# Kernel optimization log

Hardware: AMD Instinct MI355X
Metric: run time of the kernel (lower is better)

## Reference

```python
import math
import jax, jax.numpy as jnp
import numpy as np

N_HEAD = 12
LN_EPS = 1e-5

def _gelu(x):
    # NewGELU: tanh approximation
    c = math.sqrt(2.0 / math.pi)
    return 0.5 * x * (1.0 + jnp.tanh(c * (x + 0.044715 * x ** 3)))

def _ln(x, w, b):
    m = x.mean(-1, keepdims=True)
    v = x.var(-1, keepdims=True)
    return (x - m) / jnp.sqrt(v + LN_EPS) * w + b

def setup_inputs() -> dict:
    key = jax.random.key(0)
    ks = jax.random.split(key, 8)
    L, C, V, BS = 12, 768, 30522, 1024
    B, T = 4, 1024
    std = 0.02
    inp = {
        'idx': jax.random.randint(ks[0], (B, T), 0, V),
        'wte': jax.random.normal(ks[1], (V, C), jnp.float32) * std,
        'wpe': jax.random.normal(ks[2], (BS, C), jnp.float32) * std,
        'ln1_w': jnp.ones((L, C), jnp.float32),
        'ln1_b': jnp.zeros((L, C), jnp.float32),
        'attn_w': jax.random.normal(ks[3], (L, 3 * C, C), jnp.float32) * std,
        'attn_b': jnp.zeros((L, 3 * C), jnp.float32),
        'proj_w': jax.random.normal(ks[4], (L, C, C), jnp.float32) * (std / math.sqrt(2 * L)),
        'proj_b': jnp.zeros((L, C), jnp.float32),
        'ln2_w': jnp.ones((L, C), jnp.float32),
        'ln2_b': jnp.zeros((L, C), jnp.float32),
        'fc_w': jax.random.normal(ks[5], (L, 4 * C, C), jnp.float32) * std,
        'fc_b': jnp.zeros((L, 4 * C), jnp.float32),
        'mproj_w': jax.random.normal(ks[6], (L, C, 4 * C), jnp.float32) * (std / math.sqrt(2 * L)),
        'mproj_b': jnp.zeros((L, C), jnp.float32),
        'lnf_w': jnp.ones((C,), jnp.float32),
        'lnf_b': jnp.zeros((C,), jnp.float32),
        'lm_head_w': jax.random.normal(ks[7], (V, C), jnp.float32) * std,
    }
    return inp

def reference(idx, wte, wpe, ln1_w, ln1_b, attn_w, attn_b, proj_w, proj_b,
              ln2_w, ln2_b, fc_w, fc_b, mproj_w, mproj_b, lnf_w, lnf_b, lm_head_w):
    B, T = idx.shape
    C = wte.shape[1]
    H = N_HEAD
    D = C // H
    scale = 1.0 / math.sqrt(D)
    x = wte[idx] + wpe[:T][None]  # [B,T,C], drop is identity (p=0)

    def block(x, p):
        l1w, l1b, aw, ab, pw, pb, l2w, l2b, fw, fb, mw, mb = p
        h = _ln(x, l1w, l1b)
        qkv = jnp.einsum('btc,ec->bte', h, aw) + ab  # [B,T,3C]
        q, k, v = jnp.split(qkv, 3, axis=-1)
        q = q.reshape(B, T, H, D)
        k = k.reshape(B, T, H, D)
        v = v.reshape(B, T, H, D)
        att = jnp.einsum('bthd,bshd->bhts', q, k) * scale  # [B,H,T,T]
        att = jax.nn.softmax(att, axis=-1)  # mask=None: full attention
        y = jnp.einsum('bhts,bshd->bthd', att, v).reshape(B, T, C)
        x = x + jnp.einsum('btc,oc->bto', y, pw) + pb
        h = _gelu(jnp.einsum('btc,fc->btf', _ln(x, l2w, l2b), fw) + fb)
        x = x + jnp.einsum('btf,cf->btc', h, mw) + mb
        return x, None

    x, _ = jax.lax.scan(block, x, (ln1_w, ln1_b, attn_w, attn_b, proj_w, proj_b,
                                   ln2_w, ln2_b, fc_w, fc_b, mproj_w, mproj_b))
    x = _ln(x, lnf_w, lnf_b)
    logits = jnp.einsum('btc,vc->btv', x, lm_head_w)  # [B,T,V]
    return logits
```

## Files before the change

### kernel.cpp

```cpp
#include <hip/hip_runtime.h>
#include <hip/hip_bf16.h>
#include <math.h>

typedef __attribute__((ext_vector_type(8))) short short8;
typedef __attribute__((ext_vector_type(4))) float f32x4;

typedef unsigned short u16;

__device__ __forceinline__ u16 f2bf(float f) {
    union { float f; unsigned int u; } v; v.f = f;
    unsigned int u = v.u;
    unsigned int r = (u + 0x7fffu + ((u >> 16) & 1u)) >> 16;
    return (u16)r;
}
__device__ __forceinline__ float bf2f(u16 u) {
    union { unsigned int u; float f; } v; v.u = ((unsigned int)u) << 16;
    return v.f;
}

__device__ __forceinline__ void gload16(const void* g, void* l) {
    __builtin_amdgcn_global_load_lds(
        (const __attribute__((address_space(1))) void*)g,
        (__attribute__((address_space(3))) void*)l, 16, 0, 0);
}

__global__ __launch_bounds__(256) void castw_kernel(const float* __restrict__ src,
                                                    u16* __restrict__ dst,
                                                    long n, long npad) {
    long i = ((long)blockIdx.x * 256 + threadIdx.x) * 4;
    const long stride = (long)gridDim.x * 1024;
    for (; i < npad; i += stride) {
        ushort4 o;
        if (i < n) {
            float4 v = *reinterpret_cast<const float4*>(src + i);
            o.x = f2bf(v.x); o.y = f2bf(v.y); o.z = f2bf(v.z); o.w = f2bf(v.w);
        } else {
            o = make_ushort4(0, 0, 0, 0);
        }
        *reinterpret_cast<ushort4*>(dst + i) = o;
    }
}

__global__ __launch_bounds__(256) void embed_kernel(const int* __restrict__ idx,
                                                    const float* __restrict__ wte,
                                                    const float* __restrict__ wpe,
                                                    float* __restrict__ x) {
    const int row = blockIdx.x;
    const int tid = threadIdx.x;
    const int t = row & 1023;
    const int tok = idx[row];
    const float* we = wte + (size_t)tok * 768;
    const float* pe = wpe + (size_t)t * 768;
    float* xr = x + (size_t)row * 768;
    xr[tid]       = we[tid]       + pe[tid];
    xr[tid + 256] = we[tid + 256] + pe[tid + 256];
    xr[tid + 512] = we[tid + 512] + pe[tid + 512];
}

__global__ __launch_bounds__(256) void ln_kernel(const float* __restrict__ x,
                                                 const float* __restrict__ w,
                                                 const float* __restrict__ b,
                                                 u16* __restrict__ out) {
    const int wid = threadIdx.x >> 6, lane = threadIdx.x & 63;
    const int row = blockIdx.x * 4 + wid;
    const float* xr = x + (size_t)row * 768;
    const float4 v0 = *reinterpret_cast<const float4*>(xr + lane * 4);
    const float4 v1 = *reinterpret_cast<const float4*>(xr + 256 + lane * 4);
    const float4 v2 = *reinterpret_cast<const float4*>(xr + 512 + lane * 4);
    float s = v0.x + v0.y + v0.z + v0.w + v1.x + v1.y + v1.z + v1.w
            + v2.x + v2.y + v2.z + v2.w;
    float q = v0.x * v0.x + v0.y * v0.y + v0.z * v0.z + v0.w * v0.w
            + v1.x * v1.x + v1.y * v1.y + v1.z * v1.z + v1.w * v1.w
            + v2.x * v2.x + v2.y * v2.y + v2.z * v2.z + v2.w * v2.w;
    #pragma unroll
    for (int off = 32; off >= 1; off >>= 1) {
        s += __shfl_xor(s, off);
        q += __shfl_xor(q, off);
    }
    const float mean = s * (1.f / 768.f);
    const float var = q * (1.f / 768.f) - mean * mean;
    const float rstd = rsqrtf(var + 1e-5f);
    u16* orow = out + (size_t)row * 768;
    #pragma unroll
    for (int seg = 0; seg < 3; seg++) {
        const float4 v = seg == 0 ? v0 : (seg == 1 ? v1 : v2);
        const float4 wv = *reinterpret_cast<const float4*>(w + seg * 256 + lane * 4);
        const float4 bv = *reinterpret_cast<const float4*>(b + seg * 256 + lane * 4);
        ushort4 ov;
        ov.x = f2bf((v.x - mean) * rstd * wv.x + bv.x);
        ov.y = f2bf((v.y - mean) * rstd * wv.y + bv.y);
        ov.z = f2bf((v.z - mean) * rstd * wv.z + bv.z);
        ov.w = f2bf((v.w - mean) * rstd * wv.w + bv.w);
        *reinterpret_cast<ushort4*>(orow + seg * 256 + lane * 4) = ov;
    }
}

template<int EPI, int ORDER>
__global__ __launch_bounds__(512) void gemm_big(
        const u16* __restrict__ A, int lda,
        const u16* __restrict__ B, int ldb,
        const float* __restrict__ bias,
        void* __restrict__ Cout, int ldc,
        int N, int K, int nmt) {
    __shared__ __align__(16) u16 lds[2][384 * 32];
    const int tid = threadIdx.x;
    const int lane = tid & 63, wid = tid >> 6;
    const int nwg = gridDim.x;
    const int o = blockIdx.x;
    const int wg = (o & 7) * (nwg >> 3) + (o >> 3);
    int m0, n0;
    if (ORDER == 0) { m0 = (wg % nmt) * 256; n0 = (wg / nmt) * 128; }
    else            { n0 = (wg % nmt) * 128; m0 = (wg / nmt) * 256; }

    const int wm = (wid >> 1) * 64, wn = (wid & 1) * 64;
    const int l16 = lane & 15;
    const int qid = lane >> 4;
    const int xq8 = ((qid ^ (l16 & 3)) * 8);

    const int ar = tid >> 2, aq = (tid & 3) ^ (ar & 3);
    const size_t a_src0 = (size_t)(m0 + ar) * lda + aq * 8;
    const size_t a_src1 = (size_t)(m0 + ar + 128) * lda + aq * 8;
    const size_t b_src = (size_t)(n0 + ar) * ldb + aq * 8;

    f32x4 acc[4][4];
    #pragma unroll
    for (int i = 0; i < 4; i++)
        #pragma unroll
        for (int j = 0; j < 4; j++)
            acc[i][j] = (f32x4){0.f, 0.f, 0.f, 0.f};

    const int nk = K >> 5;
    gload16(A + a_src0, lds[0] + tid * 8);
    gload16(A + a_src1, lds[0] + tid * 8 + 4096);
    gload16(B + b_src,  lds[0] + tid * 8 + 8192);

    for (int t = 0; t < nk; ++t) {
        if (t + 1 < nk) {
            u16* buf = lds[(t + 1) & 1];
            const int k0 = (t + 1) << 5;
            gload16(A + a_src0 + k0, buf + tid * 8);
            gload16(A + a_src1 + k0, buf + tid * 8 + 4096);
            gload16(B + b_src + k0,  buf + tid * 8 + 8192);
            asm volatile("s_waitcnt vmcnt(3)" ::: "memory");
        } else {
            asm volatile("s_waitcnt vmcnt(0)" ::: "memory");
        }
        __builtin_amdgcn_s_barrier();
        asm volatile("" ::: "memory");
        const u16* As = lds[t & 1];
        const u16* Bs = lds[t & 1] + 8192;
        short8 af[4], bf[4];
        #pragma unroll
        for (int i = 0; i < 4; i++) {
            af[i] = *reinterpret_cast<const short8*>(&As[(wm + i * 16 + l16) * 32 + xq8]);
            bf[i] = *reinterpret_cast<const short8*>(&Bs[(wn + i * 16 + l16) * 32 + xq8]);
        }
        #pragma unroll
        for (int mi = 0; mi < 4; mi++)
            #pragma unroll
            for (int ni = 0; ni < 4; ni++)
                acc[mi][ni] = __builtin_amdgcn_mfma_f32_16x16x32_bf16(af[mi], bf[ni], acc[mi][ni], 0, 0, 0);
        asm volatile("" ::: "memory");
        __builtin_amdgcn_s_barrier();
    }

    if (EPI == 3) {
        float* ct = reinterpret_cast<float*>(&lds[0][0]) + wid * 1088;
        const int rw = (lane >> 4) * 4;
        const int rr = lane >> 2;
        const int rc = (lane & 3) * 16;
        #pragma unroll
        for (int mi = 0; mi < 4; mi++) {
            asm volatile("" ::: "memory");
            #pragma unroll
            for (int ni = 0; ni < 4; ni++)
                #pragma unroll
                for (int j = 0; j < 4; j++)
                    ct[(rw + j) * 68 + ni * 16 + l16] = acc[mi][ni][j];
            asm volatile("" ::: "memory");
            const int m = m0 + wm + mi * 16 + rr;
            const int nb = n0 + wn + rc;
            float* crow = (float*)Cout + (size_t)m * ldc + nb;
            #pragma unroll
            for (int q = 0; q < 4; q++) {
                const f32x4 v = *reinterpret_cast<const f32x4*>(&ct[rr * 68 + rc + q * 4]);
                if (nb + q * 4 + 3 < N) {
                    *reinterpret_cast<f32x4*>(crow + q * 4) = v;
                } else {
                    #pragma unroll
                    for (int e = 0; e < 4; e++)
                        if (nb + q * 4 + e < N) crow[q * 4 + e] = v[e];
                }
            }
            asm volatile("" ::: "memory");
            __builtin_amdgcn_s_barrier();
        }
    } else {
        const int cb = n0 + wn + l16;
        const int rb = m0 + wm + (lane >> 4) * 4;
        #pragma unroll
        for (int ni = 0; ni < 4; ni++) {
            const int n = cb + ni * 16;
            const float bv = bias[n];
            #pragma unroll
            for (int mi = 0; mi < 4; mi++) {
                #pragma unroll
                for (int j = 0; j < 4; j++) {
                    const int m = rb + mi * 16 + j;
                    float v = acc[mi][ni][j] + bv;
                    if (EPI == 0) {
                        ((u16*)Cout)[(size_t)m * ldc + n] = f2bf(v);
                    } else {
                        const float t = tanhf(0.7978845608028654f * (v + 0.044715f * v * v * v));
                        ((u16*)Cout)[(size_t)m * ldc + n] = f2bf(0.5f * v * (1.f + t));
                    }
                }
            }
        }
    }
}

__global__ __launch_bounds__(256) void gemm_splitk(
        const u16* __restrict__ A, int lda,
        const u16* __restrict__ B, int ldb,
        const float* __restrict__ bias,
        int ldc, int Kp, int nmt, int ntiles,
        float* __restrict__ resid) {
    __shared__ __align__(16) u16 lds[2][2][128 * 32];
    const int tid = threadIdx.x;
    const int lane = tid & 63, wid = tid >> 6;
    const int nwg = gridDim.x;
    const int o = blockIdx.x;
    const int wg = (o & 7) * (nwg >> 3) + (o >> 3);
    const int tile = wg % ntiles;
    const int ks = wg / ntiles;
    const int m0 = (tile % nmt) * 128, n0 = (tile / nmt) * 128;
    const int koff = ks * Kp;

    const int wm = (wid >> 1) * 64, wn = (wid & 1) * 64;
    const int l16 = lane & 15;
    const int qid = lane >> 4;
    const int xq8 = ((qid ^ (l16 & 3)) * 8);

    const int r0 = tid >> 2, q0 = (tid & 3) ^ (r0 & 3);
    const size_t a_src0 = (size_t)(m0 + r0) * lda + koff + q0 * 8;
    const size_t a_src1 = (size_t)(m0 + r0 + 64) * lda + koff + q0 * 8;
    const size_t b_src0 = (size_t)(n0 + r0) * ldb + koff + q0 * 8;
    const size_t b_src1 = (size_t)(n0 + r0 + 64) * ldb + koff + q0 * 8;

    f32x4 acc[4][4];
    #pragma unroll
    for (int i = 0; i < 4; i++)
        #pragma unroll
        for (int j = 0; j < 4; j++)
            acc[i][j] = (f32x4){0.f, 0.f, 0.f, 0.f};

    const int nk = Kp >> 5;
    gload16(A + a_src0, lds[0][0] + tid * 8);
    gload16(A + a_src1, lds[0][0] + tid * 8 + 2048);
    gload16(B + b_src0, lds[0][1] + tid * 8);
    gload16(B + b_src1, lds[0][1] + tid * 8 + 2048);

    for (int t = 0; t < nk; ++t) {
        if (t + 1 < nk) {
            u16* Ap = lds[(t + 1) & 1][0];
            u16* Bp = lds[(t + 1) & 1][1];
            const int k0 = (t + 1) << 5;
            gload16(A + a_src0 + k0, Ap + tid * 8);
            gload16(A + a_src1 + k0, Ap + tid * 8 + 2048);
            gload16(B + b_src0 + k0, Bp + tid * 8);
            gload16(B + b_src1 + k0, Bp + tid * 8 + 2048);
            asm volatile("s_waitcnt vmcnt(4)" ::: "memory");
        } else {
            asm volatile("s_waitcnt vmcnt(0)" ::: "memory");
        }
        __builtin_amdgcn_s_barrier();
        asm volatile("" ::: "memory");
        const u16* As = lds[t & 1][0];
        const u16* Bs = lds[t & 1][1];
        short8 af[4], bf[4];
        #pragma unroll
        for (int i = 0; i < 4; i++) {
            af[i] = *reinterpret_cast<const short8*>(&As[(wm + i * 16 + l16) * 32 + xq8]);
            bf[i] = *reinterpret_cast<const short8*>(&Bs[(wn + i * 16 + l16) * 32 + xq8]);
        }
        #pragma unroll
        for (int mi = 0; mi < 4; mi++)
            #pragma unroll
            for (int ni = 0; ni < 4; ni++)
                acc[mi][ni] = __builtin_amdgcn_mfma_f32_16x16x32_bf16(af[mi], bf[ni], acc[mi][ni], 0, 0, 0);
        asm volatile("" ::: "memory");
        __builtin_amdgcn_s_barrier();
    }

    const int cb = n0 + wn + l16;
    const int rb = m0 + wm + (lane >> 4) * 4;
    #pragma unroll
    for (int ni = 0; ni < 4; ni++) {
        const int n = cb + ni * 16;
        const float bv = (ks == 0) ? bias[n] : 0.f;
        #pragma unroll
        for (int mi = 0; mi < 4; mi++) {
            #pragma unroll
            for (int j = 0; j < 4; j++) {
                const int m = rb + mi * 16 + j;
                atomicAdd(&resid[(size_t)m * ldc + n], acc[mi][ni][j] + bv);
            }
        }
    }
}

template<int EPI>
__global__ __launch_bounds__(256, 2) void gemm_bt(
        const u16* __restrict__ A, int lda,
        const float* __restrict__ B, int ldb,
        const float* __restrict__ bias,
        void* __restrict__ Cout, int ldc,
        int M, int N, int K,
        float* __restrict__ resid) {
    __shared__ __align__(16) u16 As[128][40];
    __shared__ __align__(16) u16 Bs[128][40];
    const int tid = threadIdx.x;
    const int lane = tid & 63, wid = tid >> 6;
    const int m0 = blockIdx.y * 128, n0 = blockIdx.x * 128;
    const int wm = (wid >> 1) * 64, wn = (wid & 1) * 64;
    const int l16 = lane & 15, lk = (lane >> 4) * 8;

    f32x4 acc[4][4];
    #pragma unroll
    for (int i = 0; i < 4; i++)
        #pragma unroll
        for (int j = 0; j < 4; j++)
            acc[i][j] = (f32x4){0.f, 0.f, 0.f, 0.f};

    for (int k0 = 0; k0 < K; k0 += 32) {
        #pragma unroll
        for (int p = 0; p < 2; p++) {
            const int e = p * 256 + tid;
            const int r = e >> 2, c = e & 3;
            uint4 v = *reinterpret_cast<const uint4*>(A + (size_t)(m0 + r) * lda + k0 + c * 8);
            *reinterpret_cast<uint4*>(&As[r][c * 8]) = v;
        }
        #pragma unroll
        for (int p = 0; p < 4; p++) {
            const int e = p * 256 + tid;
            const int r = e >> 3, c = e & 7;
            float4 v = make_float4(0.f, 0.f, 0.f, 0.f);
            if (n0 + r < N)
                v = *reinterpret_cast<const float4*>(B + (size_t)(n0 + r) * ldb + k0 + c * 4);
            ushort4 hv;
            hv.x = f2bf(v.x); hv.y = f2bf(v.y); hv.z = f2bf(v.z); hv.w = f2bf(v.w);
            *reinterpret_cast<ushort4*>(&Bs[r][c * 4]) = hv;
        }
        __syncthreads();
        short8 af[4], bfr[4];
        #pragma unroll
        for (int i = 0; i < 4; i++) {
            af[i]  = *reinterpret_cast<const short8*>(&As[wm + i * 16 + l16][lk]);
            bfr[i] = *reinterpret_cast<const short8*>(&Bs[wn + i * 16 + l16][lk]);
        }
        #pragma unroll
        for (int mi = 0; mi < 4; mi++)
            #pragma unroll
            for (int ni = 0; ni < 4; ni++)
                acc[mi][ni] = __builtin_amdgcn_mfma_f32_16x16x32_bf16(af[mi], bfr[ni], acc[mi][ni], 0, 0, 0);
        __syncthreads();
    }

    const int cb = n0 + wn + l16;
    const int rb = m0 + wm + (lane >> 4) * 4;
    #pragma unroll
    for (int ni = 0; ni < 4; ni++) {
        const int n = cb + ni * 16;
        if (n >= N) continue;
        float bv = 0.f;
        if (EPI != 3) bv = bias[n];
        #pragma unroll
        for (int mi = 0; mi < 4; mi++) {
            #pragma unroll
            for (int j = 0; j < 4; j++) {
                const int m = rb + mi * 16 + j;
                float v = acc[mi][ni][j] + bv;
                if (EPI == 0) {
                    ((u16*)Cout)[(size_t)m * ldc + n] = f2bf(v);
                } else if (EPI == 1) {
                    resid[(size_t)m * ldc + n] += v;
                } else if (EPI == 2) {
                    const float t = tanhf(0.7978845608028654f * (v + 0.044715f * v * v * v));
                    ((u16*)Cout)[(size_t)m * ldc + n] = f2bf(0.5f * v * (1.f + t));
                } else {
                    ((float*)Cout)[(size_t)m * ldc + n] = v;
                }
            }
        }
    }
}

__global__ __launch_bounds__(256, 2) void attn_mfma_kernel(const u16* __restrict__ qkv,
                                                           u16* __restrict__ y) {
    __shared__ __align__(16) u16 Qs[64][72];
    __shared__ __align__(16) u16 Ks[2][64][72];
    __shared__ __align__(16) u16 Vt[2][64][72];
    __shared__ __align__(16) u16 Ps[4][16][72];

    const int tid = threadIdx.x;
    const int lane = tid & 63, wid = tid >> 6;
    const int l16 = lane & 15, lk = (lane >> 4) * 8;
    const int qt = blockIdx.x, h = blockIdx.y, b = blockIdx.z;

    const size_t base = (size_t)b * 1024 * 2304;
    const u16* qp = qkv + base + (size_t)(qt * 64) * 2304 + h * 64;
    const u16* kp = qkv + base + 768  + h * 64;
    const u16* vp = qkv + base + 1536 + h * 64;

    const int krr0 = tid >> 3, kc8_0 = tid & 7;
    const int krr1 = (tid + 256) >> 3, kc8_1 = tid & 7;
    const int vs0 = (tid >> 4) * 2, vdq0 = tid & 15;
    const int vs1 = ((tid + 256) >> 4) * 2, vdq1 = tid & 15;

    #pragma unroll
    for (int p = 0; p < 2; p++) {
        const int e = p * 256 + tid;
        const int rr = e >> 3, c8 = e & 7;
        *reinterpret_cast<uint4*>(&Qs[rr][c8 * 8]) =
            *reinterpret_cast<const uint4*>(qp + (size_t)rr * 2304 + c8 * 8);
    }
    uint4 kreg0, kreg1; ushort4 vr0a, vr0b, vr1a, vr1b;
    kreg0 = *reinterpret_cast<const uint4*>(kp + (size_t)krr0 * 2304 + kc8_0 * 8);
    kreg1 = *reinterpret_cast<const uint4*>(kp + (size_t)krr1 * 2304 + kc8_1 * 8);
    vr0a = *reinterpret_cast<const ushort4*>(vp + (size_t)vs0 * 2304 + vdq0 * 4);
    vr0b = *reinterpret_cast<const ushort4*>(vp + (size_t)(vs0 + 1) * 2304 + vdq0 * 4);
    vr1a = *reinterpret_cast<const ushort4*>(vp + (size_t)vs1 * 2304 + vdq1 * 4);
    vr1b = *reinterpret_cast<const ushort4*>(vp + (size_t)(vs1 + 1) * 2304 + vdq1 * 4);
    __syncthreads();

    short8 qf[2];
    #pragma unroll
    for (int kk = 0; kk < 2; kk++)
        qf[kk] = *reinterpret_cast<const short8*>(&Qs[wid * 16 + l16][kk * 32 + lk]);

    *reinterpret_cast<uint4*>(&Ks[0][krr0][kc8_0 * 8]) = kreg0;
    *reinterpret_cast<uint4*>(&Ks[0][krr1][kc8_1 * 8]) = kreg1;
    *reinterpret_cast<ushort2*>(&Vt[0][vdq0 * 4 + 0][vs0]) = make_ushort2(vr0a.x, vr0b.x);
    *reinterpret_cast<ushort2*>(&Vt[0][vdq0 * 4 + 1][vs0]) = make_ushort2(vr0a.y, vr0b.y);
    *reinterpret_cast<ushort2*>(&Vt[0][vdq0 * 4 + 2][vs0]) = make_ushort2(vr0a.z, vr0b.z);
    *reinterpret_cast<ushort2*>(&Vt[0][vdq0 * 4 + 3][vs0]) = make_ushort2(vr0a.w, vr0b.w);
    *reinterpret_cast<ushort2*>(&Vt[0][vdq1 * 4 + 0][vs1]) = make_ushort2(vr1a.x, vr1b.x);
    *reinterpret_cast<ushort2*>(&Vt[0][vdq1 * 4 + 1][vs1]) = make_ushort2(vr1a.y, vr1b.y);
    *reinterpret_cast<ushort2*>(&Vt[0][vdq1 * 4 + 2][vs1]) = make_ushort2(vr1a.z, vr1b.z);
    *reinterpret_cast<ushort2*>(&Vt[0][vdq1 * 4 + 3][vs1]) = make_ushort2(vr1a.w, vr1b.w);
    __syncthreads();

    f32x4 o_acc[4];
    #pragma unroll
    for (int i = 0; i < 4; i++) o_acc[i] = (f32x4){0.f, 0.f, 0.f, 0.f};
    float l_part[4] = {0.f, 0.f, 0.f, 0.f};

    for (int t = 0; t < 16; ++t) {
        const int cur = t & 1, nxt = cur ^ 1;
        if (t + 1 < 16) {
            const int s0 = (t + 1) * 64;
            kreg0 = *reinterpret_cast<const uint4*>(kp + (size_t)(s0 + krr0) * 2304 + kc8_0 * 8);
            kreg1 = *reinterpret_cast<const uint4*>(kp + (size_t)(s0 + krr1) * 2304 + kc8_1 * 8);
            vr0a = *reinterpret_cast<const ushort4*>(vp + (size_t)(s0 + vs0) * 2304 + vdq0 * 4);
            vr0b = *reinterpret_cast<const ushort4*>(vp + (size_t)(s0 + vs0 + 1) * 2304 + vdq0 * 4);
            vr1a = *reinterpret_cast<const ushort4*>(vp + (size_t)(s0 + vs1) * 2304 + vdq1 * 4);
            vr1b = *reinterpret_cast<const ushort4*>(vp + (size_t)(s0 + vs1 + 1) * 2304 + vdq1 * 4);
        }

        f32x4 sa[4];
        #pragma unroll
        for (int i = 0; i < 4; i++) sa[i] = (f32x4){0.f, 0.f, 0.f, 0.f};
        #pragma unroll
        for (int nj = 0; nj < 4; nj++) {
            #pragma unroll
            for (int kk = 0; kk < 2; kk++) {
                short8 kf = *reinterpret_cast<const short8*>(&Ks[cur][nj * 16 + l16][kk * 32 + lk]);
                sa[nj] = __builtin_amdgcn_mfma_f32_16x16x32_bf16(qf[kk], kf, sa[nj], 0, 0, 0);
            }
        }
        #pragma unroll
        for (int nj = 0; nj < 4; nj++) {
            #pragma unroll
            for (int r = 0; r < 4; r++) {
                const float pv = __expf(sa[nj][r] * 0.125f);
                l_part[r] += pv;
                Ps[wid][(lane >> 4) * 4 + r][nj * 16 + l16] = f2bf(pv);
            }
        }
        short8 pa[2];
        #pragma unroll
        for (int kk = 0; kk < 2; kk++)
            pa[kk] = *reinterpret_cast<const short8*>(&Ps[wid][l16][kk * 32 + lk]);
        #pragma unroll
        for (int nd = 0; nd < 4; nd++) {
            #pragma unroll
            for (int kk = 0; kk < 2; kk++) {
                short8 vf = *reinterpret_cast<const short8*>(&Vt[cur][nd * 16 + l16][kk * 32 + lk]);
                o_acc[nd] = __builtin_amdgcn_mfma_f32_16x16x32_bf16(pa[kk], vf, o_acc[nd], 0, 0, 0);
            }
        }

        if (t + 1 < 16) {
            *reinterpret_cast<uint4*>(&Ks[nxt][krr0][kc8_0 * 8]) = kreg0;
            *reinterpret_cast<uint4*>(&Ks[nxt][krr1][kc8_1 * 8]) = kreg1;
            *reinterpret_cast<ushort2*>(&Vt[nxt][vdq0 * 4 + 0][vs0]) = make_ushort2(vr0a.x, vr0b.x);
            *reinterpret_cast<ushort2*>(&Vt[nxt][vdq0 * 4 + 1][vs0]) = make_ushort2(vr0a.y, vr0b.y);
            *reinterpret_cast<ushort2*>(&Vt[nxt][vdq0 * 4 + 2][vs0]) = make_ushort2(vr0a.z, vr0b.z);
            *reinterpret_cast<ushort2*>(&Vt[nxt][vdq0 * 4 + 3][vs0]) = make_ushort2(vr0a.w, vr0b.w);
            *reinterpret_cast<ushort2*>(&Vt[nxt][vdq1 * 4 + 0][vs1]) = make_ushort2(vr1a.x, vr1b.x);
            *reinterpret_cast<ushort2*>(&Vt[nxt][vdq1 * 4 + 1][vs1]) = make_ushort2(vr1a.y, vr1b.y);
            *reinterpret_cast<ushort2*>(&Vt[nxt][vdq1 * 4 + 2][vs1]) = make_ushort2(vr1a.z, vr1b.z);
            *reinterpret_cast<ushort2*>(&Vt[nxt][vdq1 * 4 + 3][vs1]) = make_ushort2(vr1a.w, vr1b.w);
        }
        __syncthreads();
    }

    float inv[4];
    #pragma unroll
    for (int r = 0; r < 4; r++) {
        float s = l_part[r];
        #pragma unroll
        for (int off = 8; off >= 1; off >>= 1) s += __shfl_xor(s, off);
        inv[r] = 1.f / s;
    }
    const int rowb = b * 1024 + qt * 64 + wid * 16 + (lane >> 4) * 4;
    #pragma unroll
    for (int nd = 0; nd < 4; nd++) {
        const int col = h * 64 + nd * 16 + l16;
        #pragma unroll
        for (int r = 0; r < 4; r++) {
            y[(size_t)(rowb + r) * 768 + col] = f2bf(o_acc[nd][r] * inv[r]);
        }
    }
}

extern "C" void kernel_launch(void* const* d_in, const int* in_sizes, int n_in,
                              void* d_out, int out_size, void* d_ws, size_t ws_size,
                              hipStream_t stream) {
    (void)in_sizes; (void)n_in; (void)out_size;
    const int*   idx    = (const int*)d_in[0];
    const float* wte    = (const float*)d_in[1];
    const float* wpe    = (const float*)d_in[2];
    const float* ln1w   = (const float*)d_in[3];
    const float* ln1b   = (const float*)d_in[4];
    const float* attnw  = (const float*)d_in[5];
    const float* attnb  = (const float*)d_in[6];
    const float* projw  = (const float*)d_in[7];
    const float* projb  = (const float*)d_in[8];
    const float* ln2w   = (const float*)d_in[9];
    const float* ln2b   = (const float*)d_in[10];
    const float* fcw    = (const float*)d_in[11];
    const float* fcb    = (const float*)d_in[12];
    const float* mprojw = (const float*)d_in[13];
    const float* mprojb = (const float*)d_in[14];
    const float* lnfw   = (const float*)d_in[15];
    const float* lnfb   = (const float*)d_in[16];
    const float* lmw    = (const float*)d_in[17];
    float* out = (float*)d_out;

    char* p = (char*)d_ws;
    size_t used = 0;
    auto take = [&](size_t bytes) { char* q = p + used; used += (bytes + 255) & ~(size_t)255; return q; };
    float* x      = (float*)take((size_t)4096 * 768 * 4);
    u16*   a_bf   = (u16*)take((size_t)4096 * 768 * 2);
    u16*   qkv_bf = (u16*)take((size_t)4096 * 2304 * 2);
    u16*   hid_bf = (u16*)take((size_t)4096 * 3072 * 2);
    u16*   w_lm   = (u16*)take((size_t)30592 * 768 * 2);
    const bool castLm = used <= ws_size;
    u16*   w_attn = (u16*)take((size_t)12 * 2304 * 768 * 2);
    u16*   w_proj = (u16*)take((size_t)12 * 768 * 768 * 2);
    u16*   w_fc   = (u16*)take((size_t)12 * 3072 * 768 * 2);
    u16*   w_mprj = (u16*)take((size_t)12 * 768 * 3072 * 2);
    const bool castAll = used <= ws_size;

    embed_kernel<<<4096, 256, 0, stream>>>(idx, wte, wpe, x);

    if (castLm)
        castw_kernel<<<2048, 256, 0, stream>>>(lmw, w_lm, (long)30522 * 768, (long)30592 * 768);
    if (castAll) {
        castw_kernel<<<2048, 256, 0, stream>>>(attnw,  w_attn, (long)12 * 2304 * 768, (long)12 * 2304 * 768);
        castw_kernel<<<2048, 256, 0, stream>>>(projw,  w_proj, (long)12 * 768 * 768,  (long)12 * 768 * 768);
        castw_kernel<<<2048, 256, 0, stream>>>(fcw,    w_fc,   (long)12 * 3072 * 768, (long)12 * 3072 * 768);
        castw_kernel<<<2048, 256, 0, stream>>>(mprojw, w_mprj, (long)12 * 768 * 3072, (long)12 * 768 * 3072);
    }

    for (int l = 0; l < 12; l++) {
        ln_kernel<<<1024, 256, 0, stream>>>(x, ln1w + l * 768, ln1b + l * 768, a_bf);
        if (castAll) {
            gemm_big<0, 0><<<16 * 18, 512, 0, stream>>>(
                a_bf, 768, w_attn + (size_t)l * 2304 * 768, 768, attnb + l * 2304,
                (void*)qkv_bf, 2304, 2304, 768, 16);
        } else {
            gemm_bt<0><<<dim3(18, 32), 256, 0, stream>>>(
                a_bf, 768, attnw + (size_t)l * 2304 * 768, 768, attnb + l * 2304,
                (void*)qkv_bf, 2304, 4096, 2304, 768, nullptr);
        }
        attn_mfma_kernel<<<dim3(16, 12, 4), 256, 0, stream>>>(qkv_bf, a_bf);
        if (castAll) {
            gemm_splitk<<<192 * 2, 256, 0, stream>>>(
                a_bf, 768, w_proj + (size_t)l * 768 * 768, 768, projb + l * 768,
                768, 384, 32, 192, x);
        } else {
            gemm_bt<1><<<dim3(6, 32), 256, 0, stream>>>(
                a_bf, 768, projw + (size_t)l * 768 * 768, 768, projb + l * 768,
                nullptr, 768, 4096, 768, 768, x);
        }
        ln_kernel<<<1024, 256, 0, stream>>>(x, ln2w + l * 768, ln2b + l * 768, a_bf);
        if (castAll) {
            gemm_big<2, 0><<<16 * 24, 512, 0, stream>>>(
                a_bf, 768, w_fc + (size_t)l * 3072 * 768, 768, fcb + l * 3072,
                (void*)hid_bf, 3072, 3072, 768, 16);
            gemm_splitk<<<192 * 4, 256, 0, stream>>>(
                hid_bf, 3072, w_mprj + (size_t)l * 768 * 3072, 3072, mprojb + l * 768,
                768, 768, 32, 192, x);
        } else {
            gemm_bt<2><<<dim3(24, 32), 256, 0, stream>>>(
                a_bf, 768, fcw + (size_t)l * 3072 * 768, 768, fcb + l * 3072,
                (void*)hid_bf, 3072, 4096, 3072, 768, nullptr);
            gemm_bt<1><<<dim3(6, 32), 256, 0, stream>>>(
                hid_bf, 3072, mprojw + (size_t)l * 768 * 3072, 3072, mprojb + l * 768,
                nullptr, 768, 4096, 768, 3072, x);
        }
    }

    ln_kernel<<<1024, 256, 0, stream>>>(x, lnfw, lnfb, a_bf);
    if (castLm) {
        gemm_big<3, 1><<<16 * 239, 512, 0, stream>>>(
            a_bf, 768, w_lm, 768, nullptr, (void*)out, 30522, 30522, 768, 239);
    } else {
        gemm_bt<3><<<dim3(239, 32), 256, 0, stream>>>(
            a_bf, 768, lmw, 768, nullptr, (void*)out, 30522, 4096, 30522, 768, nullptr);
    }
}
```

Before: 3.039 ms.

## Widen attention tiles to 128 queries, retune GEMM LDS swizzle and padding

The attention kernel now processes 128 query rows per workgroup with 8 waves (512 threads), so each K/V tile loaded into LDS is shared by twice as many queries and global K/V traffic is halved. The GEMM kernels change the LDS XOR swizzle to key on row pairs instead of single rows, aimed at fewer bank conflicts with the 16x16x32 MFMA fragment reads. The EPI==3 staging stride goes from 68 to 76 floats, also to reduce bank conflicts. In exchange the attention grid has half as many workgroups (384), and larger blocks with more LDS may lower occupancy.

New measurement: 2.996 ms. No clear change (-1.4%).

```diff
diff --git a/kernel.cpp b/kernel.cpp
--- a/kernel.cpp
+++ b/kernel.cpp
@@ -115,9 +115,9 @@
     const int wm = (wid >> 1) * 64, wn = (wid & 1) * 64;
     const int l16 = lane & 15;
     const int qid = lane >> 4;
-    const int xq8 = ((qid ^ (l16 & 3)) * 8);
-
-    const int ar = tid >> 2, aq = (tid & 3) ^ (ar & 3);
+    const int xq8 = ((qid ^ ((l16 >> 1) & 3)) * 8);
+
+    const int ar = tid >> 2, aq = (tid & 3) ^ ((ar >> 1) & 3);
     const size_t a_src0 = (size_t)(m0 + ar) * lda + aq * 8;
     const size_t a_src1 = (size_t)(m0 + ar + 128) * lda + aq * 8;
     const size_t b_src = (size_t)(n0 + ar) * ldb + aq * 8;
@@ -165,7 +165,7 @@
     }
 
     if (EPI == 3) {
-        float* ct = reinterpret_cast<float*>(&lds[0][0]) + wid * 1088;
+        float* ct = reinterpret_cast<float*>(&lds[0][0]) + wid * 1216;
         const int rw = (lane >> 4) * 4;
         const int rr = lane >> 2;
         const int rc = (lane & 3) * 16;
@@ -176,14 +176,14 @@
             for (int ni = 0; ni < 4; ni++)
                 #pragma unroll
                 for (int j = 0; j < 4; j++)
-                    ct[(rw + j) * 68 + ni * 16 + l16] = acc[mi][ni][j];
+                    ct[(rw + j) * 76 + ni * 16 + l16] = acc[mi][ni][j];
             asm volatile("" ::: "memory");
             const int m = m0 + wm + mi * 16 + rr;
             const int nb = n0 + wn + rc;
             float* crow = (float*)Cout + (size_t)m * ldc + nb;
             #pragma unroll
             for (int q = 0; q < 4; q++) {
-                const f32x4 v = *reinterpret_cast<const f32x4*>(&ct[rr * 68 + rc + q * 4]);
+                const f32x4 v = *reinterpret_cast<const f32x4*>(&ct[rr * 76 + rc + q * 4]);
                 if (nb + q * 4 + 3 < N) {
                     *reinterpret_cast<f32x4*>(crow + q * 4) = v;
                 } else {
@@ -240,9 +240,9 @@
     const int wm = (wid >> 1) * 64, wn = (wid & 1) * 64;
     const int l16 = lane & 15;
     const int qid = lane >> 4;
-    const int xq8 = ((qid ^ (l16 & 3)) * 8);
-
-    const int r0 = tid >> 2, q0 = (tid & 3) ^ (r0 & 3);
+    const int xq8 = ((qid ^ ((l16 >> 1) & 3)) * 8);
+
+    const int r0 = tid >> 2, q0 = (tid & 3) ^ ((r0 >> 1) & 3);
     const size_t a_src0 = (size_t)(m0 + r0) * lda + koff + q0 * 8;
     const size_t a_src1 = (size_t)(m0 + r0 + 64) * lda + koff + q0 * 8;
     const size_t b_src0 = (size_t)(n0 + r0) * ldb + koff + q0 * 8;
@@ -396,12 +396,12 @@
     }
 }
 
-__global__ __launch_bounds__(256, 2) void attn_mfma_kernel(const u16* __restrict__ qkv,
+__global__ __launch_bounds__(512, 2) void attn_mfma_kernel(const u16* __restrict__ qkv,
                                                            u16* __restrict__ y) {
-    __shared__ __align__(16) u16 Qs[64][72];
+    __shared__ __align__(16) u16 Qs[128][72];
     __shared__ __align__(16) u16 Ks[2][64][72];
     __shared__ __align__(16) u16 Vt[2][64][72];
-    __shared__ __align__(16) u16 Ps[4][16][72];
+    __shared__ __align__(16) u16 Ps[8][16][72];
 
     const int tid = threadIdx.x;
     const int lane = tid & 63, wid = tid >> 6;
@@ -409,29 +409,24 @@
     const int qt = blockIdx.x, h = blockIdx.y, b = blockIdx.z;
 
     const size_t base = (size_t)b * 1024 * 2304;
-    const u16* qp = qkv + base + (size_t)(qt * 64) * 2304 + h * 64;
+    const u16* qp = qkv + base + (size_t)(qt * 128) * 2304 + h * 64;
     const u16* kp = qkv + base + 768  + h * 64;
     const u16* vp = qkv + base + 1536 + h * 64;
 
-    const int krr0 = tid >> 3, kc8_0 = tid & 7;
-    const int krr1 = (tid + 256) >> 3, kc8_1 = tid & 7;
-    const int vs0 = (tid >> 4) * 2, vdq0 = tid & 15;
-    const int vs1 = ((tid + 256) >> 4) * 2, vdq1 = tid & 15;
+    const int krr = tid >> 3, kc8 = tid & 7;
+    const int vs = (tid >> 4) * 2, vdq = tid & 15;
 
     #pragma unroll
     for (int p = 0; p < 2; p++) {
-        const int e = p * 256 + tid;
+        const int e = p * 512 + tid;
         const int rr = e >> 3, c8 = e & 7;
         *reinterpret_cast<uint4*>(&Qs[rr][c8 * 8]) =
             *reinterpret_cast<const uint4*>(qp + (size_t)rr * 2304 + c8 * 8);
     }
-    uint4 kreg0, kreg1; ushort4 vr0a, vr0b, vr1a, vr1b;
-    kreg0 = *reinterpret_cast<const uint4*>(kp + (size_t)krr0 * 2304 + kc8_0 * 8);
-    kreg1 = *reinterpret_cast<const uint4*>(kp + (size_t)krr1 * 2304 + kc8_1 * 8);
-    vr0a = *reinterpret_cast<const ushort4*>(vp + (size_t)vs0 * 2304 + vdq0 * 4);
-    vr0b = *reinterpret_cast<const ushort4*>(vp + (size_t)(vs0 + 1) * 2304 + vdq0 * 4);
-    vr1a = *reinterpret_cast<const ushort4*>(vp + (size_t)vs1 * 2304 + vdq1 * 4);
-    vr1b = *reinterpret_cast<const ushort4*>(vp + (size_t)(vs1 + 1) * 2304 + vdq1 * 4);
+    uint4 kreg; ushort4 vra, vrb;
+    kreg = *reinterpret_cast<const uint4*>(kp + (size_t)krr * 2304 + kc8 * 8);
+    vra = *reinterpret_cast<const ushort4*>(vp + (size_t)vs * 2304 + vdq * 4);
+    vrb = *reinterpret_cast<const ushort4*>(vp + (size_t)(vs + 1) * 2304 + vdq * 4);
     __syncthreads();
 
     short8 qf[2];
@@ -439,16 +434,11 @@
     for (int kk = 0; kk < 2; kk++)
         qf[kk] = *reinterpret_cast<const short8*>(&Qs[wid * 16 + l16][kk * 32 + lk]);
 
-    *reinterpret_cast<uint4*>(&Ks[0][krr0][kc8_0 * 8]) = kreg0;
-    *reinterpret_cast<uint4*>(&Ks[0][krr1][kc8_1 * 8]) = kreg1;
-    *reinterpret_cast<ushort2*>(&Vt[0][vdq0 * 4 + 0][vs0]) = make_ushort2(vr0a.x, vr0b.x);
-    *reinterpret_cast<ushort2*>(&Vt[0][vdq0 * 4 + 1][vs0]) = make_ushort2(vr0a.y, vr0b.y);
-    *reinterpret_cast<ushort2*>(&Vt[0][vdq0 * 4 + 2][vs0]) = make_ushort2(vr0a.z, vr0b.z);
-    *reinterpret_cast<ushort2*>(&Vt[0][vdq0 * 4 + 3][vs0]) = make_ushort2(vr0a.w, vr0b.w);
-    *reinterpret_cast<ushort2*>(&Vt[0][vdq1 * 4 + 0][vs1]) = make_ushort2(vr1a.x, vr1b.x);
-    *reinterpret_cast<ushort2*>(&Vt[0][vdq1 * 4 + 1][vs1]) = make_ushort2(vr1a.y, vr1b.y);
-    *reinterpret_cast<ushort2*>(&Vt[0][vdq1 * 4 + 2][vs1]) = make_ushort2(vr1a.z, vr1b.z);
-    *reinterpret_cast<ushort2*>(&Vt[0][vdq1 * 4 + 3][vs1]) = make_ushort2(vr1a.w, vr1b.w);
+    *reinterpret_cast<uint4*>(&Ks[0][krr][kc8 * 8]) = kreg;
+    *reinterpret_cast<ushort2*>(&Vt[0][vdq * 4 + 0][vs]) = make_ushort2(vra.x, vrb.x);
+    *reinterpret_cast<ushort2*>(&Vt[0][vdq * 4 + 1][vs]) = make_ushort2(vra.y, vrb.y);
+    *reinterpret_cast<ushort2*>(&Vt[0][vdq * 4 + 2][vs]) = make_ushort2(vra.z, vrb.z);
+    *reinterpret_cast<ushort2*>(&Vt[0][vdq * 4 + 3][vs]) = make_ushort2(vra.w, vrb.w);
     __syncthreads();
 
     f32x4 o_acc[4];
@@ -460,12 +450,9 @@
         const int cur = t & 1, nxt = cur ^ 1;
         if (t + 1 < 16) {
             const int s0 = (t + 1) * 64;
-            kreg0 = *reinterpret_cast<const uint4*>(kp + (size_t)(s0 + krr0) * 2304 + kc8_0 * 8);
-            kreg1 = *reinterpret_cast<const uint4*>(kp + (size_t)(s0 + krr1) * 2304 + kc8_1 * 8);
-            vr0a = *reinterpret_cast<const ushort4*>(vp + (size_t)(s0 + vs0) * 2304 + vdq0 * 4);
-            vr0b = *reinterpret_cast<const ushort4*>(vp + (size_t)(s0 + vs0 + 1) * 2304 + vdq0 * 4);
-            vr1a = *reinterpret_cast<const ushort4*>(vp + (size_t)(s0 + vs1) * 2304 + vdq1 * 4);
-            vr1b = *reinterpret_cast<const ushort4*>(vp + (size_t)(s0 + vs1 + 1) * 2304 + vdq1 * 4);
+            kreg = *reinterpret_cast<const uint4*>(kp + (size_t)(s0 + krr) * 2304 + kc8 * 8);
+            vra = *reinterpret_cast<const ushort4*>(vp + (size_t)(s0 + vs) * 2304 + vdq * 4);
+            vrb = *reinterpret_cast<const ushort4*>(vp + (size_t)(s0 + vs + 1) * 2304 + vdq * 4);
         }
 
         f32x4 sa[4];
@@ -502,16 +489,11 @@
         }
 
         if (t + 1 < 16) {
-            *reinterpret_cast<uint4*>(&Ks[nxt][krr0][kc8_0 * 8]) = kreg0;
-            *reinterpret_cast<uint4*>(&Ks[nxt][krr1][kc8_1 * 8]) = kreg1;
-            *reinterpret_cast<ushort2*>(&Vt[nxt][vdq0 * 4 + 0][vs0]) = make_ushort2(vr0a.x, vr0b.x);
-            *reinterpret_cast<ushort2*>(&Vt[nxt][vdq0 * 4 + 1][vs0]) = make_ushort2(vr0a.y, vr0b.y);
-            *reinterpret_cast<ushort2*>(&Vt[nxt][vdq0 * 4 + 2][vs0]) = make_ushort2(vr0a.z, vr0b.z);
-            *reinterpret_cast<ushort2*>(&Vt[nxt][vdq0 * 4 + 3][vs0]) = make_ushort2(vr0a.w, vr0b.w);
-            *reinterpret_cast<ushort2*>(&Vt[nxt][vdq1 * 4 + 0][vs1]) = make_ushort2(vr1a.x, vr1b.x);
-            *reinterpret_cast<ushort2*>(&Vt[nxt][vdq1 * 4 + 1][vs1]) = make_ushort2(vr1a.y, vr1b.y);
-            *reinterpret_cast<ushort2*>(&Vt[nxt][vdq1 * 4 + 2][vs1]) = make_ushort2(vr1a.z, vr1b.z);
-            *reinterpret_cast<ushort2*>(&Vt[nxt][vdq1 * 4 + 3][vs1]) = make_ushort2(vr1a.w, vr1b.w);
+            *reinterpret_cast<uint4*>(&Ks[nxt][krr][kc8 * 8]) = kreg;
+            *reinterpret_cast<ushort2*>(&Vt[nxt][vdq * 4 + 0][vs]) = make_ushort2(vra.x, vrb.x);
+            *reinterpret_cast<ushort2*>(&Vt[nxt][vdq * 4 + 1][vs]) = make_ushort2(vra.y, vrb.y);
+            *reinterpret_cast<ushort2*>(&Vt[nxt][vdq * 4 + 2][vs]) = make_ushort2(vra.z, vrb.z);
+            *reinterpret_cast<ushort2*>(&Vt[nxt][vdq * 4 + 3][vs]) = make_ushort2(vra.w, vrb.w);
         }
         __syncthreads();
     }
@@ -524,7 +506,7 @@
         for (int off = 8; off >= 1; off >>= 1) s += __shfl_xor(s, off);
         inv[r] = 1.f / s;
     }
-    const int rowb = b * 1024 + qt * 64 + wid * 16 + (lane >> 4) * 4;
+    const int rowb = b * 1024 + qt * 128 + wid * 16 + (lane >> 4) * 4;
     #pragma unroll
     for (int nd = 0; nd < 4; nd++) {
         const int col = h * 64 + nd * 16 + l16;
@@ -596,7 +578,7 @@
                 a_bf, 768, attnw + (size_t)l * 2304 * 768, 768, attnb + l * 2304,
                 (void*)qkv_bf, 2304, 4096, 2304, 768, nullptr);
         }
-        attn_mfma_kernel<<<dim3(16, 12, 4), 256, 0, stream>>>(qkv_bf, a_bf);
+        attn_mfma_kernel<<<dim3(8, 12, 4), 512, 0, stream>>>(qkv_bf, a_bf);
         if (castAll) {
             gemm_splitk<<<192 * 2, 256, 0, stream>>>(
                 a_bf, 768, w_proj + (size_t)l * 768 * 768, 768, projb + l * 768,
```
